# Optimization experiments

Measured on AMD Instinct MI355X. Metric: run time of the kernel, lower is better.

Reference implementation:

```python
import jax, jax.numpy as jnp
import numpy as np
import math

D, H, B, T = 1024, 16, 2, 2048
DH = D // H


def setup_inputs() -> dict:
    key = jax.random.key(0)
    ks = jax.random.split(key, 9)
    s = 1.0 / math.sqrt(D)
    x = jax.random.normal(ks[0], (B, T, D), dtype=jnp.float32)
    # True = masked position (masked_fill semantics); causal mask broadcast over b, h
    mask = jnp.triu(jnp.ones((T, T), dtype=bool), k=1)[None, None, :, :]
    wq = jax.random.normal(ks[1], (D, D), dtype=jnp.float32) * s
    bq = jnp.zeros((D,), dtype=jnp.float32)
    wk = jax.random.normal(ks[2], (D, D), dtype=jnp.float32) * s
    bk = jnp.zeros((D,), dtype=jnp.float32)
    wv = jax.random.normal(ks[3], (D, D), dtype=jnp.float32) * s
    bv = jnp.zeros((D,), dtype=jnp.float32)
    wo = jax.random.normal(ks[4], (D, D), dtype=jnp.float32) * s
    bo = jnp.zeros((D,), dtype=jnp.float32)
    return {"x": x, "mask": mask, "wq": wq, "bq": bq, "wk": wk, "bk": bk,
            "wv": wv, "bv": bv, "wo": wo, "bo": bo}


def _rotate_half(u):
    h = u.shape[-1] // 2
    return jnp.concatenate([-u[..., h:], u[..., :h]], axis=-1)


def _sincos(t, dh, dtype):
    pos = jnp.arange(t, dtype=dtype)[:, None]                    # [t, 1]
    inv = 1.0 / (10000.0 ** (jnp.arange(0, dh, 2, dtype=dtype) / dh))  # [dh/2]
    ang = pos * inv                                              # [t, dh/2]
    sin = jnp.repeat(jnp.sin(ang), 2, axis=-1)                   # [t, dh]
    cos = jnp.repeat(jnp.cos(ang), 2, axis=-1)
    return sin, cos


def reference(x, mask, wq, bq, wk, bk, wv, bv, wo, bo):
    b, t, d = x.shape
    h, dh = H, DH
    def heads(u):  # [b,t,d] -> [b,h,t,dh]
        return u.reshape(b, t, h, dh).transpose(0, 2, 1, 3)
    q = heads(x @ wq + bq)
    k = heads(x @ wk + bk)
    v = heads(x @ wv + bv)
    sin, cos = _sincos(t, dh, x.dtype)                           # [t, dh]
    q = q * cos + _rotate_half(q) * sin
    k = k * cos + _rotate_half(k) * sin
    a = jnp.einsum('bhqd,bhkd->bhqk', q, k) / jnp.sqrt(jnp.asarray(dh, x.dtype))
    a = jnp.where(mask, jnp.asarray(-10000.0, x.dtype), a)
    a = jax.nn.softmax(a, axis=-1)                               # dropout p=0.0 -> identity
    out = jnp.einsum('bhqk,bhkd->bhqd', a, v)
    out = out.transpose(0, 2, 1, 3).reshape(b, t, d)
    return out @ wo + bo
```

## Files before the change

### kernel.cpp

```cpp
#include <hip/hip_runtime.h>
#include <hip/hip_bf16.h>

#define DD 1024
#define HH 16
#define BB 2
#define TT 2048
#define DHH 64
#define MM (BB * TT)
#define NQT (TT / 64)
#define BKG 32
#define OBK 64
#define SFT 0.18033688011112042f

typedef __attribute__((ext_vector_type(8))) short bfrag;
typedef __attribute__((ext_vector_type(4))) float ffrag;

__device__ __forceinline__ unsigned short f2bf(float f) {
    __hip_bfloat16 h = __float2bfloat16(f);
    return *reinterpret_cast<unsigned short*>(&h);
}

__device__ __forceinline__ void gl_lds16(const unsigned short* g, unsigned short* l) {
    __builtin_amdgcn_global_load_lds(
        (const __attribute__((address_space(1))) unsigned int*)g,
        (__attribute__((address_space(3))) unsigned int*)l, 16, 0, 0);
}

__global__ __launch_bounds__(256) void prepass_kernel(
    const float* __restrict__ x, unsigned short* __restrict__ xb,
    const float* __restrict__ wq, const float* __restrict__ wk,
    const float* __restrict__ wv, const float* __restrict__ wo,
    unsigned short* __restrict__ oq, unsigned short* __restrict__ ok,
    unsigned short* __restrict__ ov, unsigned short* __restrict__ oo,
    float2* __restrict__ rope_tab)
{
    __shared__ float T[64][65];
    const int z = blockIdx.z;
    const int t = threadIdx.x;
    if (z == 4) {
        const int bid = blockIdx.y * 16 + blockIdx.x;
#pragma unroll
        for (int g = 0; g < 16; ++g) {
            int i = bid * 4096 + g * 256 + t;
            float4 v = ((const float4*)x)[i];
            ushort4 o;
            o.x = f2bf(v.x); o.y = f2bf(v.y); o.z = f2bf(v.z); o.w = f2bf(v.w);
            ((ushort4*)xb)[i] = o;
        }
        int idx = bid * 256 + t;
        int tpos = idx >> 5, i = idx & 31;
        float inv = __expf(-(float)i * (9.210340371976184f / 32.0f));
        float ang = (float)tpos * inv;
        float sv, cv;
        sincosf(ang, &sv, &cv);
        rope_tab[idx] = make_float2(cv, sv);
        return;
    }
    const float* W    = (z == 0) ? wq : (z == 1) ? wk : (z == 2) ? wv : wo;
    unsigned short* O = (z == 0) ? oq : (z == 1) ? ok : (z == 2) ? ov : oo;
    const float wsc   = (z == 0) ? SFT : 1.0f;
    const int n0 = blockIdx.x * 64, k0 = blockIdx.y * 64;
#pragma unroll
    for (int g = 0; g < 16; ++g) {
        int idx = g * 256 + t;
        int r = idx >> 6, c = idx & 63;
        T[c][r] = W[(size_t)(k0 + r) * DD + n0 + c];
    }
    __syncthreads();
#pragma unroll
    for (int g = 0; g < 16; ++g) {
        int idx = g * 256 + t;
        int r = idx >> 6, c = idx & 63;
        O[(size_t)(n0 + r) * DD + k0 + c] = f2bf(wsc * T[r][c]);
    }
}

__device__ __forceinline__ void gemm128(
    const unsigned short* __restrict__ X, const unsigned short* __restrict__ Wt,
    int m0, int n0, unsigned short* As, unsigned short* Bs, ffrag acc[4][4])
{
    const int t  = threadIdx.x;
    const int l  = t & 63, w = t >> 6;
    const int lm = l & 15, lq = l >> 4;
    const int wr = w >> 1, wc = w & 1;
    const int srow = l >> 2;
    const int scol = (l & 3) * 8;
#pragma unroll
    for (int m = 0; m < 4; ++m)
#pragma unroll
        for (int n = 0; n < 4; ++n) acc[m][n] = (ffrag){0.f, 0.f, 0.f, 0.f};

    for (int k0 = 0; k0 < DD; k0 += BKG) {
#pragma unroll
        for (int it = 0; it < 2; ++it) {
            const int row = (w * 2 + it) * 16 + srow;
            gl_lds16(&X [(size_t)(m0 + row) * DD + k0 + scol], &As[(w * 2 + it) * 512]);
            gl_lds16(&Wt[(size_t)(n0 + row) * DD + k0 + scol], &Bs[(w * 2 + it) * 512]);
        }
        __syncthreads();
        bfrag a[4], b[4];
#pragma unroll
        for (int m = 0; m < 4; ++m)
            a[m] = *(const bfrag*)&As[(wr * 64 + m * 16 + lm) * BKG + lq * 8];
#pragma unroll
        for (int n = 0; n < 4; ++n)
            b[n] = *(const bfrag*)&Bs[(wc * 64 + n * 16 + lm) * BKG + lq * 8];
#pragma unroll
        for (int m = 0; m < 4; ++m)
#pragma unroll
            for (int n = 0; n < 4; ++n)
                acc[m][n] = __builtin_amdgcn_mfma_f32_16x16x32_bf16(a[m], b[n], acc[m][n], 0, 0, 0);
        __syncthreads();
    }
}

__global__ __launch_bounds__(256) void qkv_rope_kernel(
    const unsigned short* __restrict__ xb,
    const unsigned short* __restrict__ wt_qkv,
    const float* __restrict__ bq, const float* __restrict__ bk,
    const float* __restrict__ bv, const float2* __restrict__ rope_tab,
    unsigned short* __restrict__ Qh, unsigned short* __restrict__ Kh,
    unsigned short* __restrict__ Vh)
{
    __shared__ __align__(16) unsigned short As[128 * BKG];
    __shared__ __align__(16) unsigned short Bs[128 * BKG];
    const int fid = (int)blockIdx.y * 24 + (int)blockIdx.x;
    const int xcd = fid & 7, jj = fid >> 3;
    const int mt  = (jj / 24) * 8 + xcd;
    const int nt  = jj % 24;
    const int n0 = nt * 128, m0 = mt * 128;
    ffrag acc[4][4];
    gemm128(xb, wt_qkv, m0, n0, As, Bs, acc);

    const int t  = threadIdx.x;
    const int l  = t & 63, w = t >> 6;
    const int lm = l & 15, lq = l >> 4;
    const int wr = w >> 1, wc = w & 1;
    const int ncol0 = n0 + wc * 64;
    const int which = ncol0 >> 10;
    const float* bias   = (which == 0) ? bq : (which == 1) ? bk : bv;
    unsigned short* Out = (which == 0) ? Qh : (which == 1) ? Kh : Vh;
    const int h = (ncol0 & 1023) >> 6;
    const float bsc = (which == 0) ? SFT : 1.0f;

    float bv4[4];
#pragma unroll
    for (int n = 0; n < 4; ++n) bv4[n] = bias[(ncol0 & 1023) + n * 16 + lm] * bsc;

#pragma unroll
    for (int m = 0; m < 4; ++m) {
#pragma unroll
        for (int r = 0; r < 4; ++r) {
            const int row  = m0 + wr * 64 + m * 16 + lq * 4 + r;
            const int b    = row >> 11;
            const int tpos = row & 2047;
            const int bh   = b * HH + h;
#pragma unroll
            for (int n = 0; n < 4; ++n) {
                const int j = n * 16 + lm;
                float val = acc[m][n][r] + bv4[n];
                float outv;
                if (which < 2) {
                    float pair = acc[m][n ^ 2][r] + bv4[n ^ 2];
                    float rh   = (j < 32) ? -pair : pair;
                    float2 cs  = rope_tab[tpos * 32 + (j >> 1)];
                    outv = val * cs.x + rh * cs.y;
                } else {
                    outv = val;
                }
                Out[((size_t)bh * TT + tpos) * DHH + j] = f2bf(outv);
            }
        }
    }
}

__global__ __launch_bounds__(256) void attn_kernel(
    const unsigned short* __restrict__ Qh, const unsigned short* __restrict__ Kh,
    const unsigned short* __restrict__ Vh, unsigned short* __restrict__ attn_out)
{
    __shared__ __align__(16) unsigned short Ks[2][64][72];
    __shared__ __align__(16) unsigned short Vt[2][64][72];

    const int fid = (int)blockIdx.y * 16 + (int)blockIdx.x;
    const int xcd = fid & 7, j = fid >> 3;
    const int bh  = ((j >> 4) << 3) + xcd;
    const int bx  = j & 15;

    const int t  = threadIdx.x;
    const int l  = t & 63, w = t >> 6;
    const int lm = l & 15, lq = l >> 4;
    const int g  = t >> 3;
    const int c0 = (t & 7) * 8;

    const unsigned short* Qb = Qh + (size_t)bh * TT * DHH;
    const unsigned short* Kb = Kh + (size_t)bh * TT * DHH;
    const unsigned short* Vb = Vh + (size_t)bh * TT * DHH;

    const bfrag onesf = (bfrag){0x3F80, 0x3F80, 0x3F80, 0x3F80,
                                0x3F80, 0x3F80, 0x3F80, 0x3F80};
    const int b = bh >> 4, h = bh & 15;
    const int srcA = (2 * (lq & 1)) * 16 + lm;
    const int srcB = srcA + 16;
    const bool sig = (lq >> 1) != 0;

#pragma unroll 1
    for (int pi = 0; pi < 2; ++pi) {
        const int qt  = (pi == 0) ? (NQT - 1 - bx) : bx;
        const int q0  = qt * 64, wm0 = q0 + w * 16;
        const int rowg = wm0 + lm;

        bfrag qf[2];
#pragma unroll
        for (int kc = 0; kc < 2; ++kc)
            qf[kc] = *(const bfrag*)&Qb[(size_t)(wm0 + lm) * DHH + kc * 32 + lq * 8];

        ffrag o[4];
#pragma unroll
        for (int s = 0; s < 4; ++s) o[s] = (ffrag){0.f, 0.f, 0.f, 0.f};
        ffrag lacc = (ffrag){0.f, 0.f, 0.f, 0.f};

        {
            uint4 ka  = *(const uint4*)&Kb[(size_t)(g) * DHH + c0];
            uint4 kb2 = *(const uint4*)&Kb[(size_t)(g + 32) * DHH + c0];
            uint4 va  = *(const uint4*)&Vb[(size_t)(2 * g) * DHH + c0];
            uint4 vb2 = *(const uint4*)&Vb[(size_t)(2 * g + 1) * DHH + c0];
            *(uint4*)&Ks[0][g][c0]      = ka;
            *(uint4*)&Ks[0][g + 32][c0] = kb2;
            const unsigned short* as = (const unsigned short*)&va;
            const unsigned short* bs = (const unsigned short*)&vb2;
#pragma unroll
            for (int jj = 0; jj < 8; ++jj) {
                unsigned int wp = (unsigned int)as[jj] | ((unsigned int)bs[jj] << 16);
                const int dh = c0 + jj;
                const int ch = (g >> 2) ^ ((dh >> 3) & 7);
                *(unsigned int*)&Vt[0][dh][ch * 8 + (g & 3) * 2] = wp;
            }
        }
        __syncthreads();

        const int nkt = qt + 1;
#pragma unroll 1
        for (int kt = 0; kt < nkt; ++kt) {
            const int cur = kt & 1;
            const bool pf = (kt < qt);
            uint4 ka, kb2, va, vb2;
            if (pf) {
                const int k1 = (kt + 1) * 64;
                ka  = *(const uint4*)&Kb[(size_t)(k1 + g) * DHH + c0];
                kb2 = *(const uint4*)&Kb[(size_t)(k1 + g + 32) * DHH + c0];
                va  = *(const uint4*)&Vb[(size_t)(k1 + 2 * g) * DHH + c0];
                vb2 = *(const uint4*)&Vb[(size_t)(k1 + 2 * g + 1) * DHH + c0];
            }
            const int k0 = kt * 64;

            float sv[4][4];
            __builtin_amdgcn_s_setprio(1);
#pragma unroll
            for (int s = 0; s < 4; ++s) {
                ffrag sa = (ffrag){0.f, 0.f, 0.f, 0.f};
#pragma unroll
                for (int kc = 0; kc < 2; ++kc) {
                    bfrag kf = *(const bfrag*)&Ks[cur][s * 16 + lm][kc * 32 + lq * 8];
                    sa = __builtin_amdgcn_mfma_f32_16x16x32_bf16(kf, qf[kc], sa, 0, 0, 0);
                }
#pragma unroll
                for (int r = 0; r < 4; ++r) sv[s][r] = sa[r];
            }
            __builtin_amdgcn_s_setprio(0);
            if (kt == qt) {
#pragma unroll
                for (int s = 0; s < 4; ++s)
#pragma unroll
                    for (int r = 0; r < 4; ++r) {
                        const int col = k0 + s * 16 + lq * 4 + r;
                        if (col > rowg) sv[s][r] = -1e30f;
                    }
            }
#pragma unroll
            for (int s = 0; s < 4; ++s)
#pragma unroll
                for (int r = 0; r < 4; ++r)
                    sv[s][r] = __builtin_amdgcn_exp2f(sv[s][r]);

            unsigned int pk[8];
#pragma unroll
            for (int s = 0; s < 4; ++s)
#pragma unroll
                for (int p = 0; p < 2; ++p)
                    asm("v_cvt_pk_bf16_f32 %0, %1, %2"
                        : "=v"(pk[s * 2 + p])
                        : "v"(sv[s][2 * p]), "v"(sv[s][2 * p + 1]));

            uint4 paw[2];
#pragma unroll
            for (int kc = 0; kc < 2; ++kc)
#pragma unroll
                for (int m = 0; m < 4; ++m) {
                    const int src = (m & 2) ? srcB : srcA;
                    unsigned int w0 = (unsigned int)__shfl((int)pk[kc * 4 + (m & 1)], src, 64);
                    unsigned int w1 = (unsigned int)__shfl((int)pk[kc * 4 + 2 + (m & 1)], src, 64);
                    ((unsigned int*)&paw[kc])[m] = sig ? w1 : w0;
                }

            __builtin_amdgcn_s_setprio(1);
#pragma unroll
            for (int kc = 0; kc < 2; ++kc) {
                bfrag pa = *(const bfrag*)&paw[kc];
#pragma unroll
                for (int s = 0; s < 4; ++s) {
                    const int ch = (kc * 4 + lq) ^ ((s * 2 + (lm >> 3)) & 7);
                    bfrag vf = *(const bfrag*)&Vt[cur][s * 16 + lm][ch * 8];
                    o[s] = __builtin_amdgcn_mfma_f32_16x16x32_bf16(pa, vf, o[s], 0, 0, 0);
                }
                lacc = __builtin_amdgcn_mfma_f32_16x16x32_bf16(pa, onesf, lacc, 0, 0, 0);
            }
            __builtin_amdgcn_s_setprio(0);

            if (pf) {
                const int nxt = cur ^ 1;
                *(uint4*)&Ks[nxt][g][c0]      = ka;
                *(uint4*)&Ks[nxt][g + 32][c0] = kb2;
                const unsigned short* as = (const unsigned short*)&va;
                const unsigned short* bs = (const unsigned short*)&vb2;
#pragma unroll
                for (int jj = 0; jj < 8; ++jj) {
                    unsigned int wp = (unsigned int)as[jj] | ((unsigned int)bs[jj] << 16);
                    const int dh = c0 + jj;
                    const int ch = (g >> 2) ^ ((dh >> 3) & 7);
                    *(unsigned int*)&Vt[nxt][dh][ch * 8 + (g & 3) * 2] = wp;
                }
            }
            __syncthreads();
        }

#pragma unroll
        for (int r = 0; r < 4; ++r) {
            const int trow = wm0 + lq * 4 + r;
            const float linv = 1.0f / lacc[r];
#pragma unroll
            for (int s = 0; s < 4; ++s) {
                float ov = o[s][r] * linv;
                attn_out[(((size_t)b * TT + trow) * HH + h) * DHH + s * 16 + lm] = f2bf(ov);
            }
        }
        __syncthreads();
    }
}

__global__ __launch_bounds__(256) void oproj_kernel(
    const unsigned short* __restrict__ attn, const unsigned short* __restrict__ wto,
    const float* __restrict__ bo, float* __restrict__ out)
{
    __shared__ __align__(16) unsigned short As[128 * OBK];
    __shared__ __align__(16) unsigned short Bs[64 * OBK];
    const int n0 = blockIdx.x * 64, m0 = blockIdx.y * 128;
    const int t  = threadIdx.x;
    const int l  = t & 63, w = t >> 6;
    const int lm = l & 15, lq = l >> 4;
    const int lrow = l >> 3;
    const int scol = ((l & 7) ^ lrow) * 8;
    const int swz  = lm & 7;

    ffrag acc[2][4];
#pragma unroll
    for (int m = 0; m < 2; ++m)
#pragma unroll
        for (int n = 0; n < 4; ++n) acc[m][n] = (ffrag){0.f, 0.f, 0.f, 0.f};

    for (int k0 = 0; k0 < DD; k0 += OBK) {
#pragma unroll
        for (int it = 0; it < 4; ++it) {
            const int rb = w * 32 + it * 8;
            gl_lds16(&attn[(size_t)(m0 + rb + lrow) * DD + k0 + scol], &As[rb * OBK]);
        }
#pragma unroll
        for (int it = 0; it < 2; ++it) {
            const int rb = w * 16 + it * 8;
            gl_lds16(&wto[(size_t)(n0 + rb + lrow) * DD + k0 + scol], &Bs[rb * OBK]);
        }
        __syncthreads();
#pragma unroll
        for (int kc = 0; kc < 2; ++kc) {
            const int ch = ((kc * 4 + lq) ^ swz) * 8;
            bfrag a[2], b[4];
#pragma unroll
            for (int m = 0; m < 2; ++m)
                a[m] = *(const bfrag*)&As[(w * 32 + m * 16 + lm) * OBK + ch];
#pragma unroll
            for (int n = 0; n < 4; ++n)
                b[n] = *(const bfrag*)&Bs[(n * 16 + lm) * OBK + ch];
#pragma unroll
            for (int m = 0; m < 2; ++m)
#pragma unroll
                for (int n = 0; n < 4; ++n)
                    acc[m][n] = __builtin_amdgcn_mfma_f32_16x16x32_bf16(a[m], b[n], acc[m][n], 0, 0, 0);
        }
        __syncthreads();
    }

#pragma unroll
    for (int n = 0; n < 4; ++n) {
        const int col = n0 + n * 16 + lm;
        const float bb = bo[col];
#pragma unroll
        for (int m = 0; m < 2; ++m)
#pragma unroll
            for (int r = 0; r < 4; ++r) {
                const int row = m0 + w * 32 + m * 16 + lq * 4 + r;
                out[(size_t)row * DD + col] = acc[m][n][r] + bb;
            }
    }
}

extern "C" void kernel_launch(void* const* d_in, const int* in_sizes, int n_in,
                              void* d_out, int out_size, void* d_ws, size_t ws_size,
                              hipStream_t stream) {
    const float* x  = (const float*)d_in[0];
    const float* wq = (const float*)d_in[2];
    const float* bq = (const float*)d_in[3];
    const float* wk = (const float*)d_in[4];
    const float* bk = (const float*)d_in[5];
    const float* wv = (const float*)d_in[6];
    const float* bv = (const float*)d_in[7];
    const float* wo = (const float*)d_in[8];
    const float* bo = (const float*)d_in[9];

    const size_t perT = (size_t)BB * HH * TT * DHH;
    const size_t perW = (size_t)DD * DD;
    unsigned short* xb   = (unsigned short*)d_ws;
    unsigned short* wtq  = xb  + perT;
    unsigned short* wtk  = wtq + perW;
    unsigned short* wtv  = wtk + perW;
    unsigned short* wto  = wtv + perW;
    unsigned short* Qh   = wto + perW;
    unsigned short* Kh   = Qh + perT;
    unsigned short* Vh   = Kh + perT;
    unsigned short* attn = Vh + perT;
    float2* rope_tab     = (float2*)(attn + perT);

    prepass_kernel<<<dim3(16, 16, 5), 256, 0, stream>>>(
        x, xb, wq, wk, wv, wo, wtq, wtk, wtv, wto, rope_tab);
    qkv_rope_kernel<<<dim3(24, 32), 256, 0, stream>>>(
        xb, wtq, bq, bk, bv, rope_tab, Qh, Kh, Vh);
    attn_kernel<<<dim3(NQT / 2, 32), 256, 0, stream>>>(Qh, Kh, Vh, attn);
    oproj_kernel<<<dim3(16, 32), 256, 0, stream>>>(attn, wto, bo, (float*)d_out);
}
```

Measured before the change: 207.4 us.

## Process two KV tiles per barrier with four-slot LDS ring in attention

The attention loop now handles two 64-key tiles per iteration. It keeps four LDS buffers for K and V and prefetches the next two tiles into registers while computing the current pair. This halves the number of __syncthreads barriers and doubles the prefetch distance, hiding more global-load latency. In exchange, LDS use per block doubles to about 73KB and register pressure rises from holding two tiles' worth of prefetched data, which may reduce occupancy.

```diff
diff --git a/kernel.cpp b/kernel.cpp
--- a/kernel.cpp
+++ b/kernel.cpp
@@ -178,8 +178,8 @@
     const unsigned short* __restrict__ Qh, const unsigned short* __restrict__ Kh,
     const unsigned short* __restrict__ Vh, unsigned short* __restrict__ attn_out)
 {
-    __shared__ __align__(16) unsigned short Ks[2][64][72];
-    __shared__ __align__(16) unsigned short Vt[2][64][72];
+    __shared__ __align__(16) unsigned short Ks[4][64][72];
+    __shared__ __align__(16) unsigned short Vt[4][64][72];
 
     const int fid = (int)blockIdx.y * 16 + (int)blockIdx.x;
     const int xcd = fid & 7, j = fid >> 3;
@@ -219,107 +219,18 @@
         for (int s = 0; s < 4; ++s) o[s] = (ffrag){0.f, 0.f, 0.f, 0.f};
         ffrag lacc = (ffrag){0.f, 0.f, 0.f, 0.f};
 
-        {
-            uint4 ka  = *(const uint4*)&Kb[(size_t)(g) * DHH + c0];
-            uint4 kb2 = *(const uint4*)&Kb[(size_t)(g + 32) * DHH + c0];
-            uint4 va  = *(const uint4*)&Vb[(size_t)(2 * g) * DHH + c0];
-            uint4 vb2 = *(const uint4*)&Vb[(size_t)(2 * g + 1) * DHH + c0];
-            *(uint4*)&Ks[0][g][c0]      = ka;
-            *(uint4*)&Ks[0][g + 32][c0] = kb2;
-            const unsigned short* as = (const unsigned short*)&va;
-            const unsigned short* bs = (const unsigned short*)&vb2;
-#pragma unroll
-            for (int jj = 0; jj < 8; ++jj) {
-                unsigned int wp = (unsigned int)as[jj] | ((unsigned int)bs[jj] << 16);
-                const int dh = c0 + jj;
-                const int ch = (g >> 2) ^ ((dh >> 3) & 7);
-                *(unsigned int*)&Vt[0][dh][ch * 8 + (g & 3) * 2] = wp;
-            }
-        }
-        __syncthreads();
-
         const int nkt = qt + 1;
-#pragma unroll 1
-        for (int kt = 0; kt < nkt; ++kt) {
-            const int cur = kt & 1;
-            const bool pf = (kt < qt);
-            uint4 ka, kb2, va, vb2;
-            if (pf) {
-                const int k1 = (kt + 1) * 64;
-                ka  = *(const uint4*)&Kb[(size_t)(k1 + g) * DHH + c0];
-                kb2 = *(const uint4*)&Kb[(size_t)(k1 + g + 32) * DHH + c0];
-                va  = *(const uint4*)&Vb[(size_t)(k1 + 2 * g) * DHH + c0];
-                vb2 = *(const uint4*)&Vb[(size_t)(k1 + 2 * g + 1) * DHH + c0];
-            }
-            const int k0 = kt * 64;
-
-            float sv[4][4];
-            __builtin_amdgcn_s_setprio(1);
-#pragma unroll
-            for (int s = 0; s < 4; ++s) {
-                ffrag sa = (ffrag){0.f, 0.f, 0.f, 0.f};
-#pragma unroll
-                for (int kc = 0; kc < 2; ++kc) {
-                    bfrag kf = *(const bfrag*)&Ks[cur][s * 16 + lm][kc * 32 + lq * 8];
-                    sa = __builtin_amdgcn_mfma_f32_16x16x32_bf16(kf, qf[kc], sa, 0, 0, 0);
-                }
-#pragma unroll
-                for (int r = 0; r < 4; ++r) sv[s][r] = sa[r];
-            }
-            __builtin_amdgcn_s_setprio(0);
-            if (kt == qt) {
-#pragma unroll
-                for (int s = 0; s < 4; ++s)
-#pragma unroll
-                    for (int r = 0; r < 4; ++r) {
-                        const int col = k0 + s * 16 + lq * 4 + r;
-                        if (col > rowg) sv[s][r] = -1e30f;
-                    }
-            }
-#pragma unroll
-            for (int s = 0; s < 4; ++s)
-#pragma unroll
-                for (int r = 0; r < 4; ++r)
-                    sv[s][r] = __builtin_amdgcn_exp2f(sv[s][r]);
-
-            unsigned int pk[8];
-#pragma unroll
-            for (int s = 0; s < 4; ++s)
-#pragma unroll
-                for (int p = 0; p < 2; ++p)
-                    asm("v_cvt_pk_bf16_f32 %0, %1, %2"
-                        : "=v"(pk[s * 2 + p])
-                        : "v"(sv[s][2 * p]), "v"(sv[s][2 * p + 1]));
-
-            uint4 paw[2];
-#pragma unroll
-            for (int kc = 0; kc < 2; ++kc)
-#pragma unroll
-                for (int m = 0; m < 4; ++m) {
-                    const int src = (m & 2) ? srcB : srcA;
-                    unsigned int w0 = (unsigned int)__shfl((int)pk[kc * 4 + (m & 1)], src, 64);
-                    unsigned int w1 = (unsigned int)__shfl((int)pk[kc * 4 + 2 + (m & 1)], src, 64);
-                    ((unsigned int*)&paw[kc])[m] = sig ? w1 : w0;
-                }
-
-            __builtin_amdgcn_s_setprio(1);
-#pragma unroll
-            for (int kc = 0; kc < 2; ++kc) {
-                bfrag pa = *(const bfrag*)&paw[kc];
-#pragma unroll
-                for (int s = 0; s < 4; ++s) {
-                    const int ch = (kc * 4 + lq) ^ ((s * 2 + (lm >> 3)) & 7);
-                    bfrag vf = *(const bfrag*)&Vt[cur][s * 16 + lm][ch * 8];
-                    o[s] = __builtin_amdgcn_mfma_f32_16x16x32_bf16(pa, vf, o[s], 0, 0, 0);
-                }
-                lacc = __builtin_amdgcn_mfma_f32_16x16x32_bf16(pa, onesf, lacc, 0, 0, 0);
-            }
-            __builtin_amdgcn_s_setprio(0);
-
-            if (pf) {
-                const int nxt = cur ^ 1;
-                *(uint4*)&Ks[nxt][g][c0]      = ka;
-                *(uint4*)&Ks[nxt][g + 32][c0] = kb2;
+
+#pragma unroll
+        for (int sub = 0; sub < 2; ++sub) {
+            if (sub < nkt) {
+                const int kr = sub * 64;
+                uint4 ka  = *(const uint4*)&Kb[(size_t)(kr + g) * DHH + c0];
+                uint4 kb2 = *(const uint4*)&Kb[(size_t)(kr + g + 32) * DHH + c0];
+                uint4 va  = *(const uint4*)&Vb[(size_t)(kr + 2 * g) * DHH + c0];
+                uint4 vb2 = *(const uint4*)&Vb[(size_t)(kr + 2 * g + 1) * DHH + c0];
+                *(uint4*)&Ks[sub][g][c0]      = ka;
+                *(uint4*)&Ks[sub][g + 32][c0] = kb2;
                 const unsigned short* as = (const unsigned short*)&va;
                 const unsigned short* bs = (const unsigned short*)&vb2;
 #pragma unroll
@@ -327,7 +238,113 @@
                     unsigned int wp = (unsigned int)as[jj] | ((unsigned int)bs[jj] << 16);
                     const int dh = c0 + jj;
                     const int ch = (g >> 2) ^ ((dh >> 3) & 7);
-                    *(unsigned int*)&Vt[nxt][dh][ch * 8 + (g & 3) * 2] = wp;
+                    *(unsigned int*)&Vt[sub][dh][ch * 8 + (g & 3) * 2] = wp;
+                }
+            }
+        }
+        __syncthreads();
+
+#pragma unroll 1
+        for (int it = 0; it < nkt; it += 2) {
+            uint4 ka[2], kb2[2], va[2], vb2[2];
+#pragma unroll
+            for (int sub = 0; sub < 2; ++sub) {
+                if (it + 2 + sub < nkt) {
+                    const int kr = (it + 2 + sub) * 64;
+                    ka [sub] = *(const uint4*)&Kb[(size_t)(kr + g) * DHH + c0];
+                    kb2[sub] = *(const uint4*)&Kb[(size_t)(kr + g + 32) * DHH + c0];
+                    va [sub] = *(const uint4*)&Vb[(size_t)(kr + 2 * g) * DHH + c0];
+                    vb2[sub] = *(const uint4*)&Vb[(size_t)(kr + 2 * g + 1) * DHH + c0];
+                }
+            }
+
+#pragma unroll
+            for (int sub = 0; sub < 2; ++sub) {
+                const int ktile = it + sub;
+                if (ktile < nkt) {
+                    const int cur = ktile & 3;
+                    const int k0 = ktile * 64;
+
+                    float sv[4][4];
+                    __builtin_amdgcn_s_setprio(1);
+#pragma unroll
+                    for (int s = 0; s < 4; ++s) {
+                        ffrag sa = (ffrag){0.f, 0.f, 0.f, 0.f};
+#pragma unroll
+                        for (int kc = 0; kc < 2; ++kc) {
+                            bfrag kf = *(const bfrag*)&Ks[cur][s * 16 + lm][kc * 32 + lq * 8];
+                            sa = __builtin_amdgcn_mfma_f32_16x16x32_bf16(kf, qf[kc], sa, 0, 0, 0);
+                        }
+#pragma unroll
+                        for (int r = 0; r < 4; ++r) sv[s][r] = sa[r];
+                    }
+                    __builtin_amdgcn_s_setprio(0);
+                    if (ktile == qt) {
+#pragma unroll
+                        for (int s = 0; s < 4; ++s)
+#pragma unroll
+                            for (int r = 0; r < 4; ++r) {
+                                const int col = k0 + s * 16 + lq * 4 + r;
+                                if (col > rowg) sv[s][r] = -1e30f;
+                            }
+                    }
+#pragma unroll
+                    for (int s = 0; s < 4; ++s)
+#pragma unroll
+                        for (int r = 0; r < 4; ++r)
+                            sv[s][r] = __builtin_amdgcn_exp2f(sv[s][r]);
+
+                    unsigned int pk[8];
+#pragma unroll
+                    for (int s = 0; s < 4; ++s)
+#pragma unroll
+                        for (int p = 0; p < 2; ++p)
+                            asm("v_cvt_pk_bf16_f32 %0, %1, %2"
+                                : "=v"(pk[s * 2 + p])
+                                : "v"(sv[s][2 * p]), "v"(sv[s][2 * p + 1]));
+
+                    uint4 paw[2];
+#pragma unroll
+                    for (int kc = 0; kc < 2; ++kc)
+#pragma unroll
+                        for (int m = 0; m < 4; ++m) {
+                            const int src = (m & 2) ? srcB : srcA;
+                            unsigned int w0 = (unsigned int)__shfl((int)pk[kc * 4 + (m & 1)], src, 64);
+                            unsigned int w1 = (unsigned int)__shfl((int)pk[kc * 4 + 2 + (m & 1)], src, 64);
+                            ((unsigned int*)&paw[kc])[m] = sig ? w1 : w0;
+                        }
+
+                    __builtin_amdgcn_s_setprio(1);
+#pragma unroll
+                    for (int kc = 0; kc < 2; ++kc) {
+                        bfrag pa = *(const bfrag*)&paw[kc];
+#pragma unroll
+                        for (int s = 0; s < 4; ++s) {
+                            const int ch = (kc * 4 + lq) ^ ((s * 2 + (lm >> 3)) & 7);
+                            bfrag vf = *(const bfrag*)&Vt[cur][s * 16 + lm][ch * 8];
+                            o[s] = __builtin_amdgcn_mfma_f32_16x16x32_bf16(pa, vf, o[s], 0, 0, 0);
+                        }
+                        lacc = __builtin_amdgcn_mfma_f32_16x16x32_bf16(pa, onesf, lacc, 0, 0, 0);
+                    }
+                    __builtin_amdgcn_s_setprio(0);
+                }
+            }
+
+#pragma unroll
+            for (int sub = 0; sub < 2; ++sub) {
+                if (it + 2 + sub < nkt) {
+                    const int nxt = (it + 2 + sub) & 3;
+                    *(uint4*)&Ks[nxt][g][c0]      = ka[sub];
+                    *(uint4*)&Ks[nxt][g + 32][c0] = kb2[sub];
+                    const unsigned short* as = (const unsigned short*)&va[sub];
+                    const unsigned short* bs = (const unsigned short*)&vb2[sub];
+#pragma unroll
+                    for (int jj = 0; jj < 8; ++jj) {
+                        unsigned int wp = (unsigned int)as[jj] | ((unsigned int)bs[jj] << 16);
+                        const int dh = c0 + jj;
+                        const int ch = (g >> 2) ^ ((dh >> 3) & 7);
+                        *(unsigned int*)&Vt[nxt][dh][ch * 8 + (g & 3) * 2] = wp;
+                    }
                 }
             }
             __syncthreads();
```

Result: slower. 236.8 us (+14.2%).
